# Performance work log

Measured on AMD Instinct MI355X. Metric: run time of the kernel, lower is better.

## Reference

```python
import jax, jax.numpy as jnp
import numpy as np

H = 1024
NS, NQ, S = 32, 64, 256
ADAPT_STEPS = 5


def _mlp_ln(x, W1, b1, W2, b2, g, be):
    # Linear -> ReLU -> Linear -> LayerNorm (dropout is identity in eval)
    h = jax.nn.relu(x @ W1 + b1) @ W2 + b2
    mu = h.mean(-1, keepdims=True)
    var = ((h - mu) ** 2).mean(-1, keepdims=True)
    return g * (h - mu) / jnp.sqrt(var + 1e-5) + be


def setup_inputs() -> dict:
    key = jax.random.key(0)
    ks = jax.random.split(key, 16)
    d = {}
    d['support_embeddings'] = jax.random.normal(ks[0], (NS, S, H), jnp.float32)
    d['query_embeddings'] = jax.random.normal(ks[1], (NQ, S, H), jnp.float32)
    d['support_labels'] = jax.random.randint(ks[2], (NS, S), 0, 3)
    w = lambda k, fi, fo: jax.random.normal(k, (fi, fo), jnp.float32) * (1.0 / np.sqrt(fi))
    # aspect_aware encoder
    d['aw_W1'] = w(ks[3], H, H); d['aw_b1'] = jnp.zeros((H,), jnp.float32)
    d['aw_W2'] = w(ks[4], H, H); d['aw_b2'] = jnp.zeros((H,), jnp.float32)
    d['aw_g'] = jnp.ones((H,), jnp.float32); d['aw_be'] = jnp.zeros((H,), jnp.float32)
    # aspect_contrastive encoder
    d['ct_W1'] = w(ks[5], H, H); d['ct_b1'] = jnp.zeros((H,), jnp.float32)
    d['ct_W2'] = w(ks[6], H, H); d['ct_b2'] = jnp.zeros((H,), jnp.float32)
    d['ct_g'] = jnp.ones((H,), jnp.float32); d['ct_be'] = jnp.zeros((H,), jnp.float32)
    # adaptation net (randomly-initialized 2-layer MLP in the torch code)
    d['ad_W1'] = w(ks[7], H, H); d['ad_b1'] = jnp.zeros((H,), jnp.float32)
    d['ad_W2'] = w(ks[8], H, H); d['ad_b2'] = jnp.zeros((H,), jnp.float32)
    # meta classifier
    d['cl_W1'] = w(ks[9], 2 * H, H); d['cl_b1'] = jnp.zeros((H,), jnp.float32)
    d['cl_W2'] = w(ks[10], H, 64); d['cl_b2'] = jnp.zeros((64,), jnp.float32)
    d['cl_W3'] = w(ks[11], 64, 3); d['cl_b3'] = jnp.zeros((3,), jnp.float32)
    return d


def reference(support_embeddings, query_embeddings, support_labels,
              aw_W1, aw_b1, aw_W2, aw_b2, aw_g, aw_be,
              ct_W1, ct_b1, ct_W2, ct_b2, ct_g, ct_be,
              ad_W1, ad_b1, ad_W2, ad_b2,
              cl_W1, cl_b1, cl_W2, cl_b2, cl_W3, cl_b3):
    # --- encode support set, build per-sentence aspect prototypes ---
    aw_s = _mlp_ln(support_embeddings, aw_W1, aw_b1, aw_W2, aw_b2, aw_g, aw_be)  # [NS,S,H]
    mask = (support_labels > 0).astype(aw_s.dtype)[..., None]                    # [NS,S,1]
    cnt = jnp.maximum(mask.sum(axis=1), 1.0)                                     # [NS,1]
    protos = (aw_s * mask).sum(axis=1) / cnt                                     # [NS,H] masked mean
    pn = protos / jnp.maximum(jnp.linalg.norm(protos, axis=-1, keepdims=True), 1e-8)

    # --- meta-adaptation: fused over all (query, token) pairs, 5 steps ---
    adapted = query_embeddings
    for _ in range(ADAPT_STEPS):
        qn = adapted / jnp.maximum(jnp.linalg.norm(adapted, axis=-1, keepdims=True), 1e-8)
        sims = jnp.einsum('qsh,ph->qsp', qn, pn)           # cosine similarities
        wts = jax.nn.softmax(sims, axis=-1)
        infl = jnp.einsum('qsp,ph->qsh', wts, protos)      # prototype influence
        adapted = jax.nn.relu((adapted + infl) @ ad_W1 + ad_b1) @ ad_W2 + ad_b2

    # --- classify adapted query tokens ---
    q_aw = _mlp_ln(adapted, aw_W1, aw_b1, aw_W2, aw_b2, aw_g, aw_be)
    q_ct = _mlp_ln(adapted, ct_W1, ct_b1, ct_W2, ct_b2, ct_g, ct_be)
    comb = jnp.concatenate([q_aw, q_ct], axis=-1)          # [NQ,S,2H]
    h = jax.nn.relu(comb @ cl_W1 + cl_b1)
    h = jax.nn.relu(h @ cl_W2 + cl_b2)
    preds = h @ cl_W3 + cl_b3                              # [NQ,S,3]
    return preds
```

## Files before the change

### kernel.cpp

```cpp
#include <hip/hip_runtime.h>
#include <hip/hip_bf16.h>

#define H 1024
#define NS 32
#define SS 256
#define T_Q 16384
#define M_S 8192

typedef __hip_bfloat16 bf16;
typedef short short8 __attribute__((ext_vector_type(8)));
typedef float floatx4 __attribute__((ext_vector_type(4)));

__device__ __forceinline__ float ldf(const bf16& v) { return __bfloat162float(v); }

__device__ __forceinline__ void split2(float v, bf16& h, bf16& l) {
  h = __float2bfloat16(v);
  l = __float2bfloat16(v - __bfloat162float(h));
}

__device__ __forceinline__ void gl2lds16(const void* g, void* l) {
  __builtin_amdgcn_global_load_lds(
      (const __attribute__((address_space(1))) unsigned int*)g,
      (__attribute__((address_space(3))) unsigned int*)l, 16, 0, 0);
}

__device__ __forceinline__ short8 ld8s(const bf16* p) { return *(const short8*)p; }

__global__ __launch_bounds__(256) void conv_split(const float* __restrict__ in,
                                                  bf16* __restrict__ oh,
                                                  bf16* __restrict__ ol, int n)
{
  int i = blockIdx.x * 256 + threadIdx.x;
  if (i < n) { bf16 h, l; split2(in[i], h, l); oh[i] = h; ol[i] = l; }
}

__global__ __launch_bounds__(256) void transpose_split(
    const float* __restrict__ W, bf16* __restrict__ Wh, bf16* __restrict__ Wl,
    int K, int N)
{
  __shared__ float t[32][33];
  int n0 = blockIdx.x * 32, k0 = blockIdx.y * 32;
  int tx = threadIdx.x & 31, ty = threadIdx.x >> 5;
#pragma unroll
  for (int i = 0; i < 32; i += 8)
    t[ty + i][tx] = W[(size_t)(k0 + ty + i) * N + (n0 + tx)];
  __syncthreads();
#pragma unroll
  for (int i = 0; i < 32; i += 8) {
    bf16 h, l; split2(t[tx][ty + i], h, l);
    size_t o = (size_t)(n0 + ty + i) * K + (k0 + tx);
    Wh[o] = h;
    if (Wl) Wl[o] = l;
  }
}

template<bool RELU, bool HASWL>
__global__ __launch_bounds__(512, 2) void gemm3p(
    const bf16* __restrict__ A0h, const bf16* __restrict__ A0l,
    const bf16* __restrict__ A1h, const bf16* __restrict__ A1l,
    const bf16* __restrict__ Wh,  const bf16* __restrict__ Wl,
    const float* __restrict__ bias,
    bf16* __restrict__ Ch, bf16* __restrict__ Cl,
    int M, int N, int K0, int Ktot)
{
  (void)M;
  __shared__ __align__(16) bf16 lds[2 * 32768];
  const int tid = threadIdx.x;
  const int w = tid >> 6, l = tid & 63;
  const int nbm = gridDim.x >> 2;
  const int lid = blockIdx.x;
  const int xcd = lid & 7, ib = lid >> 3;
  const int half = nbm >> 1;
  const int bn = xcd >> 1;
  const int bm = (xcd & 1) * half + ib;
  const int wr = w >> 2, wn = w & 3;
  const int m16 = l & 15, quad = l >> 4;
  const int srow = l & 15;
  const int scol = (l >> 4) * 8;

  floatx4 acc[8][4];
#pragma unroll
  for (int i = 0; i < 8; i++)
#pragma unroll
    for (int j = 0; j < 4; j++) { acc[i][j][0]=0.f; acc[i][j][1]=0.f; acc[i][j][2]=0.f; acc[i][j][3]=0.f; }

  const size_t raB0 = (size_t)(bn * 256 + (2 * w)     * 16 + srow) * Ktot + scol;
  const size_t raB1 = (size_t)(bn * 256 + (2 * w + 1) * 16 + srow) * Ktot + scol;
  const int aT  = ((w >> 1) & 1) + ((w >> 1) >> 1) * 8;
  const int aLo = w & 1;
  const size_t raA = (size_t)(bm * 256 + aT * 16 + srow) * H + scol;
  const int aDst = (aLo ? 8192 : 0) + aT * 512;
  size_t raBt[3]; int bDst[3]; int bLo[3];
#pragma unroll
  for (int i = 0; i < 3; i++) {
    int j = w * 3 + i;
    int idx = j >> 1;
    int tb = (idx < 6) ? (idx + 2) : (idx + 4);
    bLo[i] = j & 1;
    raBt[i] = (size_t)(bm * 256 + tb * 16 + srow) * H + scol;
    bDst[i] = (bLo[i] ? 8192 : 0) + tb * 512;
  }

  auto stage_alpha = [&](int t) {
    const int k0 = t << 5;
    const bf16 *Ah_, *Al_; int ke;
    if (k0 < K0) { Ah_ = A0h; Al_ = A0l; ke = k0; }
    else         { Ah_ = A1h; Al_ = A1l; ke = k0 - K0; }
    bf16* buf = lds + (t & 1) * 32768;
    gl2lds16(Wh + raB0 + k0, buf + 16384 + (2 * w) * 512);
    gl2lds16(Wh + raB1 + k0, buf + 16384 + (2 * w + 1) * 512);
    if (HASWL) {
      gl2lds16(Wl + raB0 + k0, buf + 24576 + (2 * w) * 512);
      gl2lds16(Wl + raB1 + k0, buf + 24576 + (2 * w + 1) * 512);
    }
    gl2lds16((aLo ? Al_ : Ah_) + raA + ke, buf + aDst);
  };
  auto stage_beta = [&](int t) {
    const int k0 = t << 5;
    const bf16 *Ah_, *Al_; int ke;
    if (k0 < K0) { Ah_ = A0h; Al_ = A0l; ke = k0; }
    else         { Ah_ = A1h; Al_ = A1l; ke = k0 - K0; }
    bf16* buf = lds + (t & 1) * 32768;
#pragma unroll
    for (int i = 0; i < 3; i++)
      gl2lds16((bLo[i] ? Al_ : Ah_) + raBt[i] + ke, buf + bDst[i]);
  };

  stage_alpha(0);
  stage_beta(0);
  asm volatile("s_waitcnt vmcnt(3)" ::: "memory");
  __builtin_amdgcn_s_barrier();

  const int la = l * 8;
  const int nT = Ktot >> 5;

#define MM3(MI, AH, AL)                                                                            \
    _Pragma("unroll")                                                                              \
    for (int nt = 0; nt < 4; nt++) {                                                               \
      acc[MI][nt] = __builtin_amdgcn_mfma_f32_16x16x32_bf16(AH, bh[nt],  acc[MI][nt], 0, 0, 0);    \
      acc[MI][nt] = __builtin_amdgcn_mfma_f32_16x16x32_bf16(AL, bh[nt],  acc[MI][nt], 0, 0, 0);    \
      if (HASWL)                                                                                   \
        acc[MI][nt] = __builtin_amdgcn_mfma_f32_16x16x32_bf16(AH, bl8[nt], acc[MI][nt], 0, 0, 0);  \
    }

  for (int t = 0; t < nT; ++t) {
    bf16* buf = lds + (t & 1) * 32768;
    const bf16* bA  = buf + (wr * 8) * 512 + la;
    const bf16* bAl = bA + 8192;
    const bf16* bB  = buf + 16384 + (wn * 4) * 512 + la;
    const bf16* bBl = bB + 8192;

    short8 bh[4], bl8[4];
#pragma unroll
    for (int nt = 0; nt < 4; nt++) bh[nt] = ld8s(bB + nt * 512);
    if (HASWL) {
#pragma unroll
      for (int nt = 0; nt < 4; nt++) bl8[nt] = ld8s(bBl + nt * 512);
    }
    short8 a0h = ld8s(bA),       a0l = ld8s(bAl);
    short8 a1h = ld8s(bA + 512), a1l = ld8s(bAl + 512);
    if (t + 1 < nT) stage_alpha(t + 1);
    __builtin_amdgcn_s_barrier();
    __builtin_amdgcn_s_setprio(1);
    MM3(0, a0h, a0l)
    MM3(1, a1h, a1l)
    __builtin_amdgcn_s_setprio(0);
    if (t + 1 < nT) {
      if (HASWL) asm volatile("s_waitcnt vmcnt(5)" ::: "memory");
      else       asm volatile("s_waitcnt vmcnt(3)" ::: "memory");
    } else {
      asm volatile("s_waitcnt vmcnt(0)" ::: "memory");
    }
    __builtin_amdgcn_s_barrier();

    short8 a2h = ld8s(bA + 1024), a2l = ld8s(bAl + 1024);
    short8 a3h = ld8s(bA + 1536), a3l = ld8s(bAl + 1536);
    if (t + 1 < nT) stage_beta(t + 1);
    __builtin_amdgcn_s_barrier();
    __builtin_amdgcn_s_setprio(1);
    MM3(2, a2h, a2l)
    MM3(3, a3h, a3l)
    __builtin_amdgcn_s_setprio(0);
    __builtin_amdgcn_s_barrier();

    short8 a4h = ld8s(bA + 2048), a4l = ld8s(bAl + 2048);
    short8 a5h = ld8s(bA + 2560), a5l = ld8s(bAl + 2560);
    __builtin_amdgcn_s_barrier();
    __builtin_amdgcn_s_setprio(1);
    MM3(4, a4h, a4l)
    MM3(5, a5h, a5l)
    __builtin_amdgcn_s_setprio(0);
    __builtin_amdgcn_s_barrier();

    short8 a6h = ld8s(bA + 3072), a6l = ld8s(bAl + 3072);
    short8 a7h = ld8s(bA + 3584), a7l = ld8s(bAl + 3584);
    __builtin_amdgcn_s_barrier();
    __builtin_amdgcn_s_setprio(1);
    MM3(6, a6h, a6l)
    MM3(7, a7h, a7l)
    __builtin_amdgcn_s_setprio(0);
    if (t + 1 < nT) asm volatile("s_waitcnt vmcnt(3)" ::: "memory");
    __builtin_amdgcn_s_barrier();
  }
#undef MM3

#pragma unroll
  for (int mt = 0; mt < 8; mt++) {
#pragma unroll
    for (int nt = 0; nt < 4; nt++) {
      int row0 = bm * 256 + wr * 128 + mt * 16 + quad * 4;
      int col  = bn * 256 + wn * 64 + nt * 16 + m16;
      float bv = bias ? bias[col] : 0.f;
#pragma unroll
      for (int r = 0; r < 4; r++) {
        float v = acc[mt][nt][r] + bv;
        if (RELU) v = fmaxf(v, 0.f);
        bf16 h, lo; split2(v, h, lo);
        size_t o = (size_t)(row0 + r) * N + col;
        Ch[o] = h; Cl[o] = lo;
      }
    }
  }
}

__global__ __launch_bounds__(256) void ln_pair(
    bf16* __restrict__ hh, bf16* __restrict__ hl,
    const float* __restrict__ g, const float* __restrict__ be)
{
  int row = blockIdx.x;
  bf16* ph = hh + (size_t)row * H;
  bf16* pl = hl + (size_t)row * H;
  int tid = threadIdx.x;
  float v[4];
  float s = 0.f, sq = 0.f;
#pragma unroll
  for (int j = 0; j < 4; j++) {
    int hi = tid + 256 * j;
    v[j] = ldf(ph[hi]) + ldf(pl[hi]);
    s += v[j]; sq += v[j] * v[j];
  }
  __shared__ float rs[256], rq[256];
  rs[tid] = s; rq[tid] = sq; __syncthreads();
  for (int o = 128; o; o >>= 1) {
    if (tid < o) { rs[tid] += rs[tid + o]; rq[tid] += rq[tid + o]; }
    __syncthreads();
  }
  float mu   = rs[0] * (1.0f / H);
  float var  = rq[0] * (1.0f / H) - mu * mu;
  float rstd = rsqrtf(var + 1e-5f);
#pragma unroll
  for (int j = 0; j < 4; j++) {
    int hi = tid + 256 * j;
    bf16 h, l; split2(g[hi] * (v[j] - mu) * rstd + be[hi], h, l);
    ph[hi] = h; pl[hi] = l;
  }
}

__global__ __launch_bounds__(256) void proto_kernel(
    const bf16* __restrict__ eh, const bf16* __restrict__ el,
    const int* __restrict__ labels, float* __restrict__ protos_out)
{
  int p = blockIdx.x;
  int tid = threadIdx.x;
  __shared__ unsigned char lbl[SS];
  lbl[tid] = (labels[p * SS + tid] > 0) ? 1 : 0;
  __syncthreads();
  float acc[4] = {0.f, 0.f, 0.f, 0.f};
  int cnt = 0;
  const bf16* bh = eh + (size_t)p * SS * H;
  const bf16* bl = el + (size_t)p * SS * H;
  for (int s = 0; s < SS; s++) {
    if (lbl[s]) {
      cnt++;
      const bf16* rh = bh + (size_t)s * H;
      const bf16* rl = bl + (size_t)s * H;
#pragma unroll
      for (int j = 0; j < 4; j++)
        acc[j] += ldf(rh[tid + 256 * j]) + ldf(rl[tid + 256 * j]);
    }
  }
  float ic = 1.0f / fmaxf((float)cnt, 1.0f);
#pragma unroll
  for (int j = 0; j < 4; j++) protos_out[p * H + tid + 256 * j] = acc[j] * ic;
}

__global__ __launch_bounds__(256) void pn_kernel(
    const float* __restrict__ protos, bf16* __restrict__ pnh, bf16* __restrict__ pnl)
{
  int p = blockIdx.x;
  int tid = threadIdx.x;
  __shared__ float red[256];
  float v[4];
  float sq = 0.f;
#pragma unroll
  for (int j = 0; j < 4; j++) { v[j] = protos[p * H + tid + 256 * j]; sq += v[j] * v[j]; }
  red[tid] = sq; __syncthreads();
  for (int o = 128; o; o >>= 1) {
    if (tid < o) red[tid] += red[tid + o];
    __syncthreads();
  }
  float inv = 1.0f / fmaxf(sqrtf(red[0]), 1e-8f);
#pragma unroll
  for (int j = 0; j < 4; j++) {
    bf16 h, l; split2(v[j] * inv, h, l);
    pnh[p * H + tid + 256 * j] = h;
    pnl[p * H + tid + 256 * j] = l;
  }
}

__global__ __launch_bounds__(256) void rownorm_pair(
    const bf16* __restrict__ hh, const bf16* __restrict__ hl, float* __restrict__ rn)
{
  int row = blockIdx.x;
  int tid = threadIdx.x;
  const bf16* ph = hh + (size_t)row * H;
  const bf16* pl = hl + (size_t)row * H;
  float s = 0.f;
#pragma unroll
  for (int j = 0; j < 4; j++) {
    float v = ldf(ph[tid + 256 * j]) + ldf(pl[tid + 256 * j]);
    s += v * v;
  }
  __shared__ float rs[256];
  rs[tid] = s; __syncthreads();
  for (int o = 128; o; o >>= 1) {
    if (tid < o) rs[tid] += rs[tid + o];
    __syncthreads();
  }
  if (tid == 0) rn[row] = 1.0f / fmaxf(sqrtf(rs[0]), 1e-8f);
}

__global__ __launch_bounds__(256) void sims_mfma(
    const bf16* __restrict__ Ah, const bf16* __restrict__ Al,
    const bf16* __restrict__ Bh, const bf16* __restrict__ Bl,
    float* __restrict__ sims)
{
  __shared__ bf16 AsH[64 * 32];
  __shared__ bf16 AsL[64 * 32];
  __shared__ bf16 BsH[32 * 32];
  __shared__ bf16 BsL[32 * 32];
  const int tid = threadIdx.x;
  const int w = tid >> 6, l = tid & 63;
  const int bm0 = blockIdx.x * 64;
  const int m16 = l & 15, quad = l >> 4;
  const int sr = l >> 2;
  const int sc = (l & 3) * 8;

  floatx4 acc[2];
#pragma unroll
  for (int nt = 0; nt < 2; nt++) { acc[nt][0]=0.f; acc[nt][1]=0.f; acc[nt][2]=0.f; acc[nt][3]=0.f; }

  for (int k0 = 0; k0 < H; k0 += 32) {
    gl2lds16(Ah + (size_t)(bm0 + w * 16 + sr) * H + k0 + sc, &AsH[w * 512]);
    gl2lds16(Al + (size_t)(bm0 + w * 16 + sr) * H + k0 + sc, &AsL[w * 512]);
    if (w < 2) gl2lds16(Bh + (size_t)(w * 16 + sr) * H + k0 + sc, &BsH[w * 512]);
    else       gl2lds16(Bl + (size_t)((w - 2) * 16 + sr) * H + k0 + sc, &BsL[(w - 2) * 512]);
    __syncthreads();

    short8 ah  = *(const short8*)&AsH[(w * 16 + m16) * 32 + quad * 8];
    short8 al8 = *(const short8*)&AsL[(w * 16 + m16) * 32 + quad * 8];
#pragma unroll
    for (int nt = 0; nt < 2; nt++) {
      short8 bh  = *(const short8*)&BsH[(nt * 16 + m16) * 32 + quad * 8];
      short8 bl8 = *(const short8*)&BsL[(nt * 16 + m16) * 32 + quad * 8];
      acc[nt] = __builtin_amdgcn_mfma_f32_16x16x32_bf16(ah,  bh,  acc[nt], 0, 0, 0);
      acc[nt] = __builtin_amdgcn_mfma_f32_16x16x32_bf16(al8, bh,  acc[nt], 0, 0, 0);
      acc[nt] = __builtin_amdgcn_mfma_f32_16x16x32_bf16(ah,  bl8, acc[nt], 0, 0, 0);
    }
    __syncthreads();
  }

#pragma unroll
  for (int nt = 0; nt < 2; nt++) {
    int col  = nt * 16 + m16;
    int row0 = bm0 + w * 16 + quad * 4;
#pragma unroll
    for (int r = 0; r < 4; r++)
      sims[(size_t)(row0 + r) * 32 + col] = acc[nt][r];
  }
}

__global__ __launch_bounds__(256) void softmax32(
    const float* __restrict__ sims, const float* __restrict__ rn,
    float* __restrict__ wts)
{
  int t = blockIdx.x * 8 + (threadIdx.x >> 5);
  int p = threadIdx.x & 31;
  float s = sims[(size_t)t * 32 + p] * rn[t];
  float m = s;
#pragma unroll
  for (int o = 16; o; o >>= 1) m = fmaxf(m, __shfl_xor(m, o, 64));
  float e = __expf(s - m);
  float sum = e;
#pragma unroll
  for (int o = 16; o; o >>= 1) sum += __shfl_xor(sum, o, 64);
  wts[(size_t)t * 32 + p] = e / sum;
}

__global__ __launch_bounds__(256) void infl16(
    const bf16* __restrict__ ah, const bf16* __restrict__ al,
    const float* __restrict__ wts, const float* __restrict__ protos,
    bf16* __restrict__ oh, bf16* __restrict__ ol)
{
  int t0 = blockIdx.x * 16;
  int tid = threadIdx.x;
  __shared__ float wl[16][32];
  for (int i = tid; i < 512; i += 256)
    wl[i >> 5][i & 31] = wts[(size_t)(t0 + (i >> 5)) * 32 + (i & 31)];
  __syncthreads();
  int c0 = tid * 4;
  float acc[16][4];
#pragma unroll
  for (int tk = 0; tk < 16; tk++) {
    const bf16* rh = ah + (size_t)(t0 + tk) * H + c0;
    const bf16* rl = al + (size_t)(t0 + tk) * H + c0;
#pragma unroll
    for (int j = 0; j < 4; j++) acc[tk][j] = ldf(rh[j]) + ldf(rl[j]);
  }
  for (int p = 0; p < 32; p++) {
    float4 pv = *(const float4*)&protos[p * H + c0];
#pragma unroll
    for (int tk = 0; tk < 16; tk++) {
      float w = wl[tk][p];
      acc[tk][0] += w * pv.x; acc[tk][1] += w * pv.y;
      acc[tk][2] += w * pv.z; acc[tk][3] += w * pv.w;
    }
  }
#pragma unroll
  for (int tk = 0; tk < 16; tk++) {
    bf16* wh = oh + (size_t)(t0 + tk) * H + c0;
    bf16* wo = ol + (size_t)(t0 + tk) * H + c0;
#pragma unroll
    for (int j = 0; j < 4; j++) { bf16 h, lo; split2(acc[tk][j], h, lo); wh[j] = h; wo[j] = lo; }
  }
}

__global__ __launch_bounds__(256) void gemm_small(
    const bf16* __restrict__ Ah, const bf16* __restrict__ Al,
    const float* __restrict__ W, const float* __restrict__ bias,
    float* __restrict__ C, int M, int N, int K)
{
  const int BK = 16;
  __shared__ float As[BK][64];
  __shared__ float Bs[BK][64];
  int tid = threadIdx.x;
  int tx = tid & 15, ty = tid >> 4;
  int bn0 = blockIdx.x * 64;
  int bm0 = blockIdx.y * 64;
  float acc[4][4] = {};
  int am = tid >> 2, ak = (tid & 3) * 4;
  int bk = tid >> 4, bn = (tid & 15) * 4;
  const bf16* Aph = Ah + (size_t)(bm0 + am) * K + ak;
  const bf16* Apl = Al + (size_t)(bm0 + am) * K + ak;
  const float* Wptr = W + (size_t)bk * N + bn0 + bn;
  for (int k0 = 0; k0 < K; k0 += BK) {
#pragma unroll
    for (int c = 0; c < 4; c++) As[ak + c][am] = ldf(Aph[c]) + ldf(Apl[c]);
#pragma unroll
    for (int c = 0; c < 4; c++) Bs[bk][bn + c] = Wptr[c];
    __syncthreads();
#pragma unroll
    for (int k = 0; k < BK; k++) {
      float a[4], b[4];
#pragma unroll
      for (int i = 0; i < 4; i++) a[i] = As[k][ty * 4 + i];
#pragma unroll
      for (int j = 0; j < 4; j++) b[j] = Bs[k][tx * 4 + j];
#pragma unroll
      for (int i = 0; i < 4; i++)
#pragma unroll
        for (int j = 0; j < 4; j++)
          acc[i][j] += a[i] * b[j];
    }
    __syncthreads();
    Aph += BK; Apl += BK;
    Wptr += (size_t)BK * N;
  }
#pragma unroll
  for (int i = 0; i < 4; i++) {
    float* Crow = C + (size_t)(bm0 + ty * 4 + i) * N + bn0;
#pragma unroll
    for (int j = 0; j < 4; j++) {
      int n = tx * 4 + j;
      Crow[n] = fmaxf(acc[i][j] + bias[bn0 + n], 0.f);
    }
  }
}

__global__ __launch_bounds__(256) void FewShotABSALearner_46935402610855_kernel(
    const float* __restrict__ h2, const float* __restrict__ W3,
    const float* __restrict__ b3, float* __restrict__ out,
    int t0, int nElem, int out_size)
{
  int idx = blockIdx.x * 256 + threadIdx.x;
  if (idx >= nElem) return;
  int t = idx / 3, c = idx - t * 3;
  float acc = b3[c];
  const float* hr = h2 + (size_t)t * 64;
#pragma unroll
  for (int k = 0; k < 64; k++) acc += hr[k] * W3[k * 3 + c];
  int oi = t0 * 3 + idx;
  if (oi < out_size) out[oi] = acc;
}

extern "C" void kernel_launch(void* const* d_in, const int* in_sizes, int n_in,
                              void* d_out, int out_size, void* d_ws, size_t ws_size,
                              hipStream_t stream)
{
  (void)in_sizes; (void)n_in;
  const float* sup   = (const float*)d_in[0];
  const float* qry   = (const float*)d_in[1];
  const int*   lab   = (const int*)d_in[2];
  const float *aw_W1 = (const float*)d_in[3],  *aw_b1 = (const float*)d_in[4];
  const float *aw_W2 = (const float*)d_in[5],  *aw_b2 = (const float*)d_in[6];
  const float *aw_g  = (const float*)d_in[7],  *aw_be = (const float*)d_in[8];
  const float *ct_W1 = (const float*)d_in[9],  *ct_b1 = (const float*)d_in[10];
  const float *ct_W2 = (const float*)d_in[11], *ct_b2 = (const float*)d_in[12];
  const float *ct_g  = (const float*)d_in[13], *ct_be = (const float*)d_in[14];
  const float *ad_W1 = (const float*)d_in[15], *ad_b1 = (const float*)d_in[16];
  const float *ad_W2 = (const float*)d_in[17], *ad_b2 = (const float*)d_in[18];
  const float *cl_W1 = (const float*)d_in[19], *cl_b1 = (const float*)d_in[20];
  const float *cl_W2 = (const float*)d_in[21], *cl_b2 = (const float*)d_in[22];
  const float *cl_W3 = (const float*)d_in[23], *cl_b3 = (const float*)d_in[24];
  float* out = (float*)d_out;

  const size_t MB = 1 << 20;
  int C; bool clLo = true;
  if      (ws_size >= (size_t)239403008) C = 16384;
  else if (ws_size >= (size_t)136609792) C = 8192;
  else if (ws_size >= (size_t)85213184)  C = 4096;
  else if (ws_size >= (size_t)59514880)  C = 2048;
  else if (ws_size >= (size_t)46665728)  C = 1024;
  else { C = 1024; clLo = false; }
  const int Cs = (C < M_S) ? C : M_S;
  const size_t actB = (size_t)C * H * sizeof(bf16);

  char* ws = (char*)d_ws;
  size_t off = 0;
  auto nxt = [&](size_t b) { char* p = ws + off; off += b; return p; };
  bf16* sqw[12];
  for (int i = 0; i < 12; i++) sqw[i] = (bf16*)nxt(2 * MB);
  bf16 *aw1h = sqw[0], *aw1l = sqw[1], *aw2h = sqw[2],  *aw2l = sqw[3];
  bf16 *ct1h = sqw[4], *ct1l = sqw[5], *ct2h = sqw[6],  *ct2l = sqw[7];
  bf16 *ad1h = sqw[8], *ad1l = sqw[9], *ad2h = sqw[10], *ad2l = sqw[11];
  bf16* clW1h = (bf16*)nxt(4 * MB);
  bf16* clW1l = clLo ? (bf16*)nxt(4 * MB) : nullptr;
  float* protos = (float*)nxt(NS * H * 4);
  bf16*  pnh    = (bf16*)nxt(NS * H * 2);
  bf16*  pnl    = (bf16*)nxt(NS * H * 2);
  char*  ub     = nxt((size_t)C * 256);
  float* h2c   = (float*)ub;
  float* simsb = (float*)ub;
  float* wtsb  = (float*)(ub + (size_t)C * 128);
  float* rn    = (float*)nxt((size_t)C * 4);
  bf16 *R0h = (bf16*)nxt(actB), *R0l = (bf16*)nxt(actB);
  bf16 *R1h = (bf16*)nxt(actB), *R1l = (bf16*)nxt(actB);
  bf16 *R2h = (bf16*)nxt(actB), *R2l = (bf16*)nxt(actB);

  dim3 blk(256);
  dim3 blk2(512);
  dim3 tg(32, 32);
  dim3 ggq((C / 256) * 4);
  dim3 ggs((Cs / 256) * 4);

  transpose_split<<<tg, blk, 0, stream>>>(aw_W1, aw1h, aw1l, H, H);
  transpose_split<<<tg, blk, 0, stream>>>(aw_W2, aw2h, aw2l, H, H);
  transpose_split<<<tg, blk, 0, stream>>>(ct_W1, ct1h, ct1l, H, H);
  transpose_split<<<tg, blk, 0, stream>>>(ct_W2, ct2h, ct2l, H, H);
  transpose_split<<<tg, blk, 0, stream>>>(ad_W1, ad1h, ad1l, H, H);
  transpose_split<<<tg, blk, 0, stream>>>(ad_W2, ad2h, ad2l, H, H);
  transpose_split<<<dim3(32, 64), blk, 0, stream>>>(cl_W1, clW1h, clW1l, 2 * H, H);

  for (int sc = 0; sc < M_S / Cs; sc++) {
    conv_split<<<(Cs * H) / 256, blk, 0, stream>>>(sup + (size_t)sc * Cs * H, R0h, R0l, Cs * H);
    gemm3p<true , true><<<ggs, blk2, 0, stream>>>(R0h, R0l, R0h, R0l, aw1h, aw1l, aw_b1, R1h, R1l, Cs, H, H, H);
    gemm3p<false, true><<<ggs, blk2, 0, stream>>>(R1h, R1l, R1h, R1l, aw2h, aw2l, aw_b2, R2h, R2l, Cs, H, H, H);
    ln_pair<<<Cs, blk, 0, stream>>>(R2h, R2l, aw_g, aw_be);
    proto_kernel<<<Cs / SS, blk, 0, stream>>>(R2h, R2l, lab + sc * Cs,
                                              protos + (size_t)sc * (Cs / SS) * H);
  }
  pn_kernel<<<NS, blk, 0, stream>>>(protos, pnh, pnl);

  for (int qc = 0; qc < T_Q / C; qc++) {
    const float* q0 = qry + (size_t)qc * C * H;
    conv_split<<<(C * H) / 256, blk, 0, stream>>>(q0, R2h, R2l, C * H);
    for (int it = 0; it < 5; it++) {
      rownorm_pair<<<C, blk, 0, stream>>>(R2h, R2l, rn);
      sims_mfma<<<C / 64, blk, 0, stream>>>(R2h, R2l, pnh, pnl, simsb);
      softmax32<<<C / 8, blk, 0, stream>>>(simsb, rn, wtsb);
      infl16<<<C / 16, blk, 0, stream>>>(R2h, R2l, wtsb, protos, R0h, R0l);
      gemm3p<true , true><<<ggq, blk2, 0, stream>>>(R0h, R0l, R0h, R0l, ad1h, ad1l, ad_b1, R1h, R1l, C, H, H, H);
      gemm3p<false, true><<<ggq, blk2, 0, stream>>>(R1h, R1l, R1h, R1l, ad2h, ad2l, ad_b2, R2h, R2l, C, H, H, H);
    }
    gemm3p<true , true><<<ggq, blk2, 0, stream>>>(R2h, R2l, R2h, R2l, aw1h, aw1l, aw_b1, R0h, R0l, C, H, H, H);
    gemm3p<false, true><<<ggq, blk2, 0, stream>>>(R0h, R0l, R0h, R0l, aw2h, aw2l, aw_b2, R1h, R1l, C, H, H, H);
    ln_pair<<<C, blk, 0, stream>>>(R1h, R1l, aw_g, aw_be);
    gemm3p<true , true><<<ggq, blk2, 0, stream>>>(R2h, R2l, R2h, R2l, ct1h, ct1l, ct_b1, R0h, R0l, C, H, H, H);
    gemm3p<false, true><<<ggq, blk2, 0, stream>>>(R0h, R0l, R0h, R0l, ct2h, ct2l, ct_b2, R2h, R2l, C, H, H, H);
    ln_pair<<<C, blk, 0, stream>>>(R2h, R2l, ct_g, ct_be);
    if (clLo)
      gemm3p<true, true ><<<ggq, blk2, 0, stream>>>(R1h, R1l, R2h, R2l, clW1h, clW1l, cl_b1, R0h, R0l, C, H, H, 2 * H);
    else
      gemm3p<true, false><<<ggq, blk2, 0, stream>>>(R1h, R1l, R2h, R2l, clW1h, nullptr, cl_b1, R0h, R0l, C, H, H, 2 * H);
    gemm_small<<<dim3(1, C / 64), blk, 0, stream>>>(R0h, R0l, cl_W2, cl_b2, h2c, C, 64, H);
    FewShotABSALearner_46935402610855_kernel<<<(C * 3 + 255) / 256, blk, 0, stream>>>(
        h2c, cl_W3, cl_b3, out, qc * C, C * 3, out_size);
  }
}
```

Baseline: 2.484 ms.

## Software-pipeline LDS fragment loads across MFMA phases and reduce barriers in split-bf16 GEMM

Restructures the GEMM main loop so LDS fragment reads for the next pair of M-subtiles are issued before the MFMAs of the current pair. B fragments and the first A fragments of the next K-tile are preloaded at the end of each iteration. The number of barriers per K-step drops from eight to four. This should hide LDS latency behind MFMA work, at the cost of more live registers and a full vmcnt(0) wait at the prologue and at each iteration end.

```diff
diff --git a/kernel.cpp b/kernel.cpp
--- a/kernel.cpp
+++ b/kernel.cpp
@@ -77,6 +77,7 @@
   const int m16 = l & 15, quad = l >> 4;
   const int srow = l & 15;
   const int scol = (l >> 4) * 8;
+  const int la = l * 8;
 
   floatx4 acc[8][4];
 #pragma unroll
@@ -128,10 +129,24 @@
 
   stage_alpha(0);
   stage_beta(0);
-  asm volatile("s_waitcnt vmcnt(3)" ::: "memory");
+  asm volatile("s_waitcnt vmcnt(0)" ::: "memory");
   __builtin_amdgcn_s_barrier();
 
-  const int la = l * 8;
+  short8 bh[4], bl8[4];
+  short8 s0h[2], s0l[2], s1h[2], s1l[2];
+  {
+    const bf16* bB = lds + 16384 + wn * 2048 + la;
+#pragma unroll
+    for (int nt = 0; nt < 4; nt++) bh[nt] = ld8s(bB + nt * 512);
+    if (HASWL) {
+#pragma unroll
+      for (int nt = 0; nt < 4; nt++) bl8[nt] = ld8s(bB + 8192 + nt * 512);
+    }
+    const bf16* bA = lds + wr * 4096 + la;
+    s0h[0] = ld8s(bA);        s0h[1] = ld8s(bA + 512);
+    s0l[0] = ld8s(bA + 8192); s0l[1] = ld8s(bA + 8704);
+  }
+
   const int nT = Ktot >> 5;
 
 #define MM3(MI, AH, AL)                                                                            \
@@ -144,62 +159,55 @@
     }
 
   for (int t = 0; t < nT; ++t) {
-    bf16* buf = lds + (t & 1) * 32768;
-    const bf16* bA  = buf + (wr * 8) * 512 + la;
-    const bf16* bAl = bA + 8192;
-    const bf16* bB  = buf + 16384 + (wn * 4) * 512 + la;
-    const bf16* bBl = bB + 8192;
-
-    short8 bh[4], bl8[4];
-#pragma unroll
-    for (int nt = 0; nt < 4; nt++) bh[nt] = ld8s(bB + nt * 512);
-    if (HASWL) {
-#pragma unroll
-      for (int nt = 0; nt < 4; nt++) bl8[nt] = ld8s(bBl + nt * 512);
-    }
-    short8 a0h = ld8s(bA),       a0l = ld8s(bAl);
-    short8 a1h = ld8s(bA + 512), a1l = ld8s(bAl + 512);
+    const bf16* buf  = lds + (t & 1) * 32768;
+    const bf16* nbuf = lds + ((t + 1) & 1) * 32768;
+    const bf16* bA   = buf + wr * 4096 + la;
+    const bf16* bAl  = bA + 8192;
+
     if (t + 1 < nT) stage_alpha(t + 1);
+    s1h[0] = ld8s(bA + 1024);  s1h[1] = ld8s(bA + 1536);
+    s1l[0] = ld8s(bAl + 1024); s1l[1] = ld8s(bAl + 1536);
+    __builtin_amdgcn_s_setprio(1);
+    MM3(0, s0h[0], s0l[0])
+    MM3(1, s0h[1], s0l[1])
+    __builtin_amdgcn_s_setprio(0);
     __builtin_amdgcn_s_barrier();
+
+    if (t + 1 < nT) stage_beta(t + 1);
+    s0h[0] = ld8s(bA + 2048);  s0h[1] = ld8s(bA + 2560);
+    s0l[0] = ld8s(bAl + 2048); s0l[1] = ld8s(bAl + 2560);
     __builtin_amdgcn_s_setprio(1);
-    MM3(0, a0h, a0l)
-    MM3(1, a1h, a1l)
+    MM3(2, s1h[0], s1l[0])
+    MM3(3, s1h[1], s1l[1])
+    __builtin_amdgcn_s_setprio(0);
+    __builtin_amdgcn_s_barrier();
+
+    s1h[0] = ld8s(bA + 3072);  s1h[1] = ld8s(bA + 3584);
+    s1l[0] = ld8s(bAl + 3072); s1l[1] = ld8s(bAl + 3584);
+    __builtin_amdgcn_s_setprio(1);
+    MM3(4, s0h[0], s0l[0])
+    MM3(5, s0h[1], s0l[1])
+    __builtin_amdgcn_s_setprio(0);
+    if (t + 1 < nT) asm volatile("s_waitcnt vmcnt(3)" ::: "memory");
+    __builtin_amdgcn_s_barrier();
+
+    __builtin_amdgcn_s_setprio(1);
+    MM3(6, s1h[0], s1l[0])
+    MM3(7, s1h[1], s1l[1])
     __builtin_amdgcn_s_setprio(0);
     if (t + 1 < nT) {
-      if (HASWL) asm volatile("s_waitcnt vmcnt(5)" ::: "memory");
-      else       asm volatile("s_waitcnt vmcnt(3)" ::: "memory");
-    } else {
+      const bf16* nbB = nbuf + 16384 + wn * 2048 + la;
+      const bf16* nbA = nbuf + wr * 4096 + la;
+#pragma unroll
+      for (int nt = 0; nt < 4; nt++) bh[nt] = ld8s(nbB + nt * 512);
+      if (HASWL) {
+#pragma unroll
+        for (int nt = 0; nt < 4; nt++) bl8[nt] = ld8s(nbB + 8192 + nt * 512);
+      }
+      s0h[0] = ld8s(nbA);        s0h[1] = ld8s(nbA + 512);
+      s0l[0] = ld8s(nbA + 8192); s0l[1] = ld8s(nbA + 8704);
       asm volatile("s_waitcnt vmcnt(0)" ::: "memory");
     }
-    __builtin_amdgcn_s_barrier();
-
-    short8 a2h = ld8s(bA + 1024), a2l = ld8s(bAl + 1024);
-    short8 a3h = ld8s(bA + 1536), a3l = ld8s(bAl + 1536);
-    if (t + 1 < nT) stage_beta(t + 1);
-    __builtin_amdgcn_s_barrier();
-    __builtin_amdgcn_s_setprio(1);
-    MM3(2, a2h, a2l)
-    MM3(3, a3h, a3l)
-    __builtin_amdgcn_s_setprio(0);
-    __builtin_amdgcn_s_barrier();
-
-    short8 a4h = ld8s(bA + 2048), a4l = ld8s(bAl + 2048);
-    short8 a5h = ld8s(bA + 2560), a5l = ld8s(bAl + 2560);
-    __builtin_amdgcn_s_barrier();
-    __builtin_amdgcn_s_setprio(1);
-    MM3(4, a4h, a4l)
-    MM3(5, a5h, a5l)
-    __builtin_amdgcn_s_setprio(0);
-    __builtin_amdgcn_s_barrier();
-
-    short8 a6h = ld8s(bA + 3072), a6l = ld8s(bAl + 3072);
-    short8 a7h = ld8s(bA + 3584), a7l = ld8s(bAl + 3584);
-    __builtin_amdgcn_s_barrier();
-    __builtin_amdgcn_s_setprio(1);
-    MM3(6, a6h, a6l)
-    MM3(7, a7h, a7l)
-    __builtin_amdgcn_s_setprio(0);
-    if (t + 1 < nT) asm volatile("s_waitcnt vmcnt(3)" ::: "memory");
     __builtin_amdgcn_s_barrier();
   }
 #undef MM3
```

Result: faster. 2.425 ms (-2.4%).
